# Performance work log

Hardware: AMD Instinct MI355X
Metric: run time of the kernel (lower is better)

The kernel has to match this reference:

```python
import jax, jax.numpy as jnp
import numpy as np

B, L, D, H = 8, 1024, 512, 8  # batch, seq, d_model, n_head (per-head dim == d_model)
EPS = 1e-6


def setup_inputs() -> dict:
    key = jax.random.key(0)
    ks = jax.random.split(key, 7)
    s = 1.0 / np.sqrt(D)
    return {
        "q": jax.random.normal(ks[0], (B, L, D), jnp.float32),
        "k": jax.random.normal(ks[1], (B, L, D), jnp.float32),
        "v": jax.random.normal(ks[2], (B, L, D), jnp.float32),
        "w_q": jax.random.normal(ks[3], (D, H * D), jnp.float32) * s,
        "w_k": jax.random.normal(ks[4], (D, H * D), jnp.float32) * s,
        "w_v": jax.random.normal(ks[5], (D, H * D), jnp.float32) * s,
        "w_fc": jax.random.normal(ks[6], (H * D, D), jnp.float32) * (1.0 / np.sqrt(H * D)),
        "ln_gamma": jnp.ones((D,), jnp.float32),
        "ln_beta": jnp.zeros((D,), jnp.float32),
    }


def reference(q, k, v, w_q, w_k, w_v, w_fc, ln_gamma, ln_beta):
    residual = q
    # projections -> (B, H, L, D); dropout is identity in eval mode
    qh = (q @ w_q).reshape(B, L, H, D).transpose(0, 2, 1, 3)
    kh = (k @ w_k).reshape(B, L, H, D).transpose(0, 2, 1, 3)
    vh = (v @ w_v).reshape(B, L, H, D).transpose(0, 2, 1, 3)
    temp = jnp.asarray(D, qh.dtype) ** 0.5
    scores = jnp.einsum("bhqd,bhkd->bhqk", qh / temp, kh)
    attn = jax.nn.softmax(scores, axis=-1)
    ctx = jnp.einsum("bhqk,bhkd->bhqd", attn, vh)
    ctx = ctx.transpose(0, 2, 1, 3).reshape(B, L, H * D)
    out = ctx @ w_fc + residual
    mu = jnp.mean(out, axis=-1, keepdims=True)
    var = jnp.var(out, axis=-1, keepdims=True)
    out = (out - mu) * jax.lax.rsqrt(var + EPS) * ln_gamma + ln_beta
    return out, attn
```

## Files before the change

### kernel.cpp

```cpp
#include <hip/hip_runtime.h>
#include <hip/hip_bf16.h>
#include <math.h>

typedef __bf16 bf16_t;
typedef __bf16 bf16x8 __attribute__((ext_vector_type(8)));
typedef __bf16 bf16x4 __attribute__((ext_vector_type(4)));
typedef float  f32x4  __attribute__((ext_vector_type(4)));

#define B_   8
#define L_   1024
#define D_   512
#define H_   8
#define HD_  4096
#define BL_  8192

__device__ __forceinline__ void gload_lds16(const bf16_t* g, bf16_t* l) {
  __builtin_amdgcn_global_load_lds(
      (const __attribute__((address_space(1))) unsigned int*)g,
      (__attribute__((address_space(3))) unsigned int*)l,
      16, 0, 0);
}

__global__ void f2b3(const float4* __restrict__ q, const float4* __restrict__ k,
                     const float4* __restrict__ v, bf16x4* __restrict__ qo,
                     bf16x4* __restrict__ ko, bf16x4* __restrict__ vo, int n4) {
  int i = blockIdx.x * blockDim.x + threadIdx.x;
  if (i >= n4) return;
  const float4* s = (blockIdx.y == 0) ? q : (blockIdx.y == 1) ? k : v;
  bf16x4* d = (blockIdx.y == 0) ? qo : (blockIdx.y == 1) ? ko : vo;
  float4 x = s[i];
  bf16x4 o;
  o[0] = (bf16_t)x.x; o[1] = (bf16_t)x.y; o[2] = (bf16_t)x.z; o[3] = (bf16_t)x.w;
  d[i] = o;
}

__global__ void tconv4(const float* __restrict__ wq, const float* __restrict__ wk,
                       const float* __restrict__ wv, const float* __restrict__ wfc,
                       bf16_t* __restrict__ wqT, bf16_t* __restrict__ wkT,
                       bf16_t* __restrict__ wvT, bf16_t* __restrict__ wfT) {
  __shared__ float t[32][33];
  const int z = blockIdx.z;
  const float* s; bf16_t* d; int R, C, c0, r0;
  if (z < 3) {
    s = (z == 0) ? wq : (z == 1) ? wk : wv;
    d = (z == 0) ? wqT : (z == 1) ? wkT : wvT;
    R = D_; C = HD_; c0 = blockIdx.x * 32; r0 = blockIdx.y * 32;
  } else {
    s = wfc; d = wfT;
    R = HD_; C = D_; c0 = blockIdx.y * 32; r0 = blockIdx.x * 32;
  }
  int tx = threadIdx.x, ty = threadIdx.y;
  #pragma unroll
  for (int i = 0; i < 32; i += 8)
    t[ty + i][tx] = s[(long)(r0 + ty + i) * C + c0 + tx];
  __syncthreads();
  #pragma unroll
  for (int i = 0; i < 32; i += 8)
    d[(long)(c0 + ty + i) * R + r0 + tx] = (bf16_t)t[tx][ty + i];
}

#define VM4 asm volatile("s_waitcnt vmcnt(4)" ::: "memory")
#define VM0 asm volatile("s_waitcnt vmcnt(0)" ::: "memory")

#define STG(OP, BUF, KK, TILE) do { \
  const bf16_t* gsrc_ = (OP) ? Bg : Ag; \
  const long gld_ = (OP) ? ldb : lda; \
  bf16_t* lb_ = lds + (BUF)*32768 + (OP)*16384 + (KK)*8192 + wid*512; \
  gload_lds16(gsrc_ + (long)(TILE)*64 + (KK)*32, lb_); \
  gload_lds16(gsrc_ + (long)128*gld_ + (long)(TILE)*64 + (KK)*32, lb_ + 4096); \
} while (0)

#define LDA(I, BUF, KK) (*(const bf16x8*)(lds + (BUF)*32768 + (KK)*8192 + offA[I]))
#define LDB(J, BUF, KK) (*(const bf16x8*)(lds + (BUF)*32768 + 16384 + (KK)*8192 + offB[J]))

#define MM(q, ii, jj) acc[(q)*4+(ii)][(jj)] = \
  __builtin_amdgcn_mfma_f32_16x16x32_bf16(a##ii, b##jj, acc[(q)*4+(ii)][(jj)], 0, 0, 0)

#define PHASE(Q, KK, BUF, STAGE, VM) do { \
  bf16x8 a0, a1, a2, a3; \
  if ((Q) == 0) { b0 = LDB(0,BUF,KK); b1 = LDB(1,BUF,KK); b2 = LDB(2,BUF,KK); b3 = LDB(3,BUF,KK); } \
  a0 = LDA((Q)*4+0,BUF,KK); a1 = LDA((Q)*4+1,BUF,KK); \
  a2 = LDA((Q)*4+2,BUF,KK); a3 = LDA((Q)*4+3,BUF,KK); \
  STAGE; \
  __builtin_amdgcn_s_barrier(); \
  asm volatile("s_waitcnt lgkmcnt(0)" ::: "memory"); \
  __builtin_amdgcn_sched_barrier(0); \
  __builtin_amdgcn_s_setprio(1); \
  MM(Q,0,0); MM(Q,1,0); MM(Q,2,0); MM(Q,3,0); \
  MM(Q,0,1); MM(Q,1,1); MM(Q,2,1); MM(Q,3,1); \
  MM(Q,0,2); MM(Q,1,2); MM(Q,2,2); MM(Q,3,2); \
  MM(Q,0,3); MM(Q,1,3); MM(Q,2,3); MM(Q,3,3); \
  __builtin_amdgcn_s_setprio(0); \
  VM; \
  __builtin_amdgcn_s_barrier(); \
} while (0)

template<int EPI>
__launch_bounds__(512, 2)
__global__ void gemm256(const bf16_t* __restrict__ A, long sAb, long sAh, int lda,
                        const bf16_t* __restrict__ Bt, long sBb, long sBh, int ldb,
                        void* __restrict__ Cv, long sCb, long sCh, int ldc,
                        int K, float scale)
{
  __shared__ __align__(16) bf16_t lds[65536];
  const int bz = blockIdx.z, b = bz >> 3, h = bz & 7;
  A  += (long)b * sAb + (long)h * sAh;
  Bt += (long)b * sBb + (long)h * sBh;
  const int m0 = blockIdx.y * 256, n0 = blockIdx.x * 256;
  const int tid = threadIdx.x, lane = tid & 63, wid = tid >> 6;
  const int wm = wid >> 2, wn = wid & 3;

  const int srow  = tid >> 2;
  const int sslot = (lane & 3) ^ ((tid >> 3) & 3);
  const bf16_t* Ag = A + (long)(m0 + srow) * lda + sslot * 8;
  const bf16_t* Bg = Bt + (long)(n0 + srow) * ldb + sslot * 8;

  int offA[8], offB[4];
  #pragma unroll
  for (int i = 0; i < 8; ++i) {
    const int r = wm * 128 + i * 16 + (lane & 15);
    offA[i] = r * 32 + (((lane >> 4) ^ ((r >> 1) & 3)) * 8);
  }
  #pragma unroll
  for (int j = 0; j < 4; ++j) {
    const int r = wn * 64 + j * 16 + (lane & 15);
    offB[j] = r * 32 + (((lane >> 4) ^ ((r >> 1) & 3)) * 8);
  }

  f32x4 acc[8][4] = {};
  const int ITER = K >> 7;

  STG(0,0,0,0); STG(0,0,1,0); STG(1,0,0,0); STG(1,0,1,0);
  STG(0,1,0,1); STG(1,1,0,1);
  VM4;
  __builtin_amdgcn_s_barrier();

  for (int i = 0; i < ITER; ++i) {
    const int t = 2 * i;
    const bool stg = (i + 1 < ITER);
    bf16x8 b0, b1, b2, b3;
    PHASE(0,0,0, STG(0,1,1,t+1);                , (void)0);
    PHASE(1,0,0, STG(1,1,1,t+1);                , (void)0);
    PHASE(0,1,0, { if (stg) STG(0,0,0,t+2); }   , (void)0);
    PHASE(1,1,0, { if (stg) STG(1,0,0,t+2); }   , { if (stg) { VM4; } else { VM0; } });
    PHASE(0,0,1, { if (stg) STG(0,0,1,t+2); }   , (void)0);
    PHASE(1,0,1, { if (stg) STG(1,0,1,t+2); }   , (void)0);
    PHASE(0,1,1, { if (stg) STG(0,1,0,t+3); }   , (void)0);
    PHASE(1,1,1, { if (stg) STG(1,1,0,t+3); }   , { if (stg) { VM4; } });
  }

  const long coff = (long)b * sCb + (long)h * sCh;
  #pragma unroll
  for (int i = 0; i < 8; ++i) {
    const int rbase = m0 + wm * 128 + i * 16 + ((lane >> 4) << 2);
    #pragma unroll
    for (int j = 0; j < 4; ++j) {
      const int c = n0 + wn * 64 + j * 16 + (lane & 15);
      if (EPI == 3) {
        const int b2 = rbase >> 10, l2 = rbase & 1023;
        const int h2 = c >> 9, d2 = c & 511;
        bf16x4 o4;
        #pragma unroll
        for (int r = 0; r < 4; ++r) o4[r] = (bf16_t)(acc[i][j][r] * scale);
        *(bf16x4*)((bf16_t*)Cv + (long)(b2 * 8 + h2) * D_ * L_ + (long)d2 * L_ + l2) = o4;
      } else {
        #pragma unroll
        for (int r = 0; r < 4; ++r) {
          float vv = acc[i][j][r] * scale;
          long idx = coff + (long)(rbase + r) * ldc + c;
          if (EPI == 0) ((bf16_t*)Cv)[idx] = (bf16_t)vv;
          else          ((float*)Cv)[idx] = vv;
        }
      }
    }
  }
}

template<int BM, int BN, int EPI>
__launch_bounds__(256, 2)
__global__ void gemm_bt(const bf16_t* __restrict__ A, long sAb, long sAh, int lda,
                        const bf16_t* __restrict__ Bt, long sBb, long sBh, int ldb,
                        void* __restrict__ Cv, long sCb, long sCh, int ldc,
                        int K, float scale, const float* __restrict__ res)
{
  constexpr int WN    = (BN == 128) ? 2 : 1;
  constexpr int SPANM = BM / (4 / WN);
  constexpr int MI    = SPANM / 16;
  constexpr int NJ    = 4;
  __shared__ bf16_t sA[BM * 64];
  __shared__ bf16_t sB[BN * 64];
  const int bz = blockIdx.z, b = bz >> 3, h = bz & 7;
  A  += (long)b * sAb + (long)h * sAh;
  Bt += (long)b * sBb + (long)h * sBh;
  const int m0 = blockIdx.y * BM, n0 = blockIdx.x * BN;
  const int tid = threadIdx.x, lane = tid & 63, wid = tid >> 6;
  const int waveM = (WN == 2) ? (wid >> 1) : wid;
  const int waveN = (WN == 2) ? (wid & 1) : 0;
  f32x4 acc[MI][NJ] = {};
  const int srow = wid * 8 + (lane >> 3);
  const int skin = (lane & 7) * 8;
  const bf16_t* Ag = A + (long)(m0 + srow) * lda + skin;
  const bf16_t* Bg = Bt + (long)(n0 + srow) * ldb + skin;
  for (int k0 = 0; k0 < K; k0 += 64) {
    #pragma unroll
    for (int j = 0; j < BM / 32; ++j)
      gload_lds16(Ag + (long)(j * 32) * lda + k0, sA + (j * 4 + wid) * 512);
    #pragma unroll
    for (int j = 0; j < BN / 32; ++j)
      gload_lds16(Bg + (long)(j * 32) * ldb + k0, sB + (j * 4 + wid) * 512);
    __syncthreads();
    #pragma unroll
    for (int kk = 0; kk < 2; ++kk) {
      bf16x8 af[MI], bfr[NJ];
      #pragma unroll
      for (int i = 0; i < MI; ++i)
        af[i]  = *(const bf16x8*)(sA + (waveM * SPANM + i * 16 + (lane & 15)) * 64 + kk * 32 + ((lane >> 4) * 8));
      #pragma unroll
      for (int j = 0; j < NJ; ++j)
        bfr[j] = *(const bf16x8*)(sB + (waveN * 64 + j * 16 + (lane & 15)) * 64 + kk * 32 + ((lane >> 4) * 8));
      #pragma unroll
      for (int i = 0; i < MI; ++i)
        #pragma unroll
        for (int j = 0; j < NJ; ++j)
          acc[i][j] = __builtin_amdgcn_mfma_f32_16x16x32_bf16(af[i], bfr[j], acc[i][j], 0, 0, 0);
    }
    __syncthreads();
  }
  const long coff = (long)b * sCb + (long)h * sCh;
  #pragma unroll
  for (int i = 0; i < MI; ++i) {
    const int rbase = m0 + waveM * SPANM + i * 16 + ((lane >> 4) << 2);
    #pragma unroll
    for (int j = 0; j < NJ; ++j) {
      const int c = n0 + waveN * 64 + j * 16 + (lane & 15);
      #pragma unroll
      for (int r = 0; r < 4; ++r) {
        float v = acc[i][j][r] * scale;
        long idx = coff + (long)(rbase + r) * ldc + c;
        if (EPI == 0)      ((bf16_t*)Cv)[idx] = (bf16_t)v;
        else if (EPI == 1) ((float*)Cv)[idx] = v;
        else               ((float*)Cv)[idx] = v + res[(long)(rbase + r) * ldc + c];
      }
    }
  }
}

__global__ void softmax_bf16(bf16_t* __restrict__ braw, float* __restrict__ attn) {
  const long row = (long)blockIdx.x * 4 + (threadIdx.x >> 6);
  const int lane = threadIdx.x & 63;
  bf16_t* p = braw + row * 1024;
  float* ao = attn + row * 1024;
  float v[16];
  float m = -1e30f;
  #pragma unroll
  for (int j = 0; j < 4; ++j) {
    bf16x4 x = *(const bf16x4*)(p + j * 256 + lane * 4);
    #pragma unroll
    for (int e = 0; e < 4; ++e) {
      v[j * 4 + e] = (float)x[e];
      m = fmaxf(m, v[j * 4 + e]);
    }
  }
  #pragma unroll
  for (int o = 32; o; o >>= 1) m = fmaxf(m, __shfl_xor(m, o));
  float s = 0.f;
  #pragma unroll
  for (int e = 0; e < 16; ++e) { v[e] = __expf(v[e] - m); s += v[e]; }
  #pragma unroll
  for (int o = 32; o; o >>= 1) s += __shfl_xor(s, o);
  const float inv = 1.f / s;
  #pragma unroll
  for (int j = 0; j < 4; ++j) {
    float4 f; bf16x4 o4;
    f.x = v[j*4+0] * inv; f.y = v[j*4+1] * inv;
    f.z = v[j*4+2] * inv; f.w = v[j*4+3] * inv;
    o4[0] = (bf16_t)f.x; o4[1] = (bf16_t)f.y; o4[2] = (bf16_t)f.z; o4[3] = (bf16_t)f.w;
    ((float4*)ao)[j * 64 + lane] = f;
    *(bf16x4*)(p + j * 256 + lane * 4) = o4;
  }
}

__global__ void softmax_rows(float* __restrict__ attn, bf16_t* __restrict__ abf) {
  const long row = (long)blockIdx.x * 4 + (threadIdx.x >> 6);
  const int lane = threadIdx.x & 63;
  float* p = attn + row * 1024;
  float4 v[4];
  float m = -1e30f;
  #pragma unroll
  for (int j = 0; j < 4; ++j) {
    v[j] = ((const float4*)p)[j * 64 + lane];
    m = fmaxf(m, fmaxf(fmaxf(v[j].x, v[j].y), fmaxf(v[j].z, v[j].w)));
  }
  #pragma unroll
  for (int o = 32; o; o >>= 1) m = fmaxf(m, __shfl_xor(m, o));
  float s = 0.f;
  #pragma unroll
  for (int j = 0; j < 4; ++j) {
    v[j].x = expf(v[j].x - m); v[j].y = expf(v[j].y - m);
    v[j].z = expf(v[j].z - m); v[j].w = expf(v[j].w - m);
    s += v[j].x + v[j].y + v[j].z + v[j].w;
  }
  #pragma unroll
  for (int o = 32; o; o >>= 1) s += __shfl_xor(s, o);
  const float inv = 1.f / s;
  bf16x4* ab = (bf16x4*)(abf + row * 1024);
  #pragma unroll
  for (int j = 0; j < 4; ++j) {
    v[j].x *= inv; v[j].y *= inv; v[j].z *= inv; v[j].w *= inv;
    ((float4*)p)[j * 64 + lane] = v[j];
    bf16x4 o4;
    o4[0] = (bf16_t)v[j].x; o4[1] = (bf16_t)v[j].y;
    o4[2] = (bf16_t)v[j].z; o4[3] = (bf16_t)v[j].w;
    ab[j * 64 + lane] = o4;
  }
}

__global__ void ln_rows(float* __restrict__ o, const float* __restrict__ g,
                        const float* __restrict__ be) {
  const long row = (long)blockIdx.x * 4 + (threadIdx.x >> 6);
  const int lane = threadIdx.x & 63;
  float* p = o + row * 512;
  float4 a = ((const float4*)p)[lane];
  float4 b = ((const float4*)p)[lane + 64];
  float s  = a.x + a.y + a.z + a.w + b.x + b.y + b.z + b.w;
  float s2 = a.x*a.x + a.y*a.y + a.z*a.z + a.w*a.w
           + b.x*b.x + b.y*b.y + b.z*b.z + b.w*b.w;
  #pragma unroll
  for (int t = 32; t; t >>= 1) { s += __shfl_xor(s, t); s2 += __shfl_xor(s2, t); }
  const float mu  = s * (1.f / 512.f);
  const float var = s2 * (1.f / 512.f) - mu * mu;
  const float inv = rsqrtf(var + 1e-6f);
  float4 g0 = ((const float4*)g)[lane],  g1 = ((const float4*)g)[lane + 64];
  float4 b0 = ((const float4*)be)[lane], b1 = ((const float4*)be)[lane + 64];
  a.x = (a.x - mu) * inv * g0.x + b0.x;  a.y = (a.y - mu) * inv * g0.y + b0.y;
  a.z = (a.z - mu) * inv * g0.z + b0.z;  a.w = (a.w - mu) * inv * g0.w + b0.w;
  b.x = (b.x - mu) * inv * g1.x + b1.x;  b.y = (b.y - mu) * inv * g1.y + b1.y;
  b.z = (b.z - mu) * inv * g1.z + b1.z;  b.w = (b.w - mu) * inv * g1.w + b1.w;
  ((float4*)p)[lane] = a;
  ((float4*)p)[lane + 64] = b;
}

extern "C" void kernel_launch(void* const* d_in, const int* in_sizes, int n_in,
                              void* d_out, int out_size, void* d_ws, size_t ws_size,
                              hipStream_t stream) {
  const float* q   = (const float*)d_in[0];
  const float* k   = (const float*)d_in[1];
  const float* v   = (const float*)d_in[2];
  const float* wq  = (const float*)d_in[3];
  const float* wk  = (const float*)d_in[4];
  const float* wv  = (const float*)d_in[5];
  const float* wfc = (const float*)d_in[6];
  const float* lng = (const float*)d_in[7];
  const float* lnb = (const float*)d_in[8];

  float* out   = (float*)d_out;
  float* attnf = out + (long)BL_ * D_;

  char* ws = (char*)d_ws;
  const long MB = 1024 * 1024;
  bf16_t* qbf = (bf16_t*)(ws +   0 * MB);
  bf16_t* kbf = (bf16_t*)(ws +   8 * MB);
  bf16_t* vbf = (bf16_t*)(ws +  16 * MB);
  bf16_t* wqT = (bf16_t*)(ws +  24 * MB);
  bf16_t* wkT = (bf16_t*)(ws +  28 * MB);
  bf16_t* wvT = (bf16_t*)(ws +  32 * MB);
  bf16_t* wfT = (bf16_t*)(ws +  36 * MB);
  bf16_t* qh  = (bf16_t*)(ws +  40 * MB);
  bf16_t* kh  = (bf16_t*)(ws + 104 * MB);
  bf16_t* vh  = (bf16_t*)(ws + 168 * MB);
  bf16_t* vhT = (bf16_t*)(ws + 232 * MB);
  bf16_t* ctx = vh;

  const bool fused = (ws_size >= (size_t)(424 * MB));
  bf16_t* braw = (bf16_t*)(ws + 296 * MB);
  bf16_t* abf  = fused ? braw : qh;

  const int n4 = BL_ * D_ / 4;
  f2b3<<<dim3(n4 / 256, 3), 256, 0, stream>>>((const float4*)q, (const float4*)k,
                                              (const float4*)v, (bf16x4*)qbf,
                                              (bf16x4*)kbf, (bf16x4*)vbf, n4);
  tconv4<<<dim3(128, 16, 4), dim3(32, 8), 0, stream>>>(wq, wk, wv, wfc,
                                                       wqT, wkT, wvT, wfT);

  const float qscale = 1.0f / sqrtf((float)D_);
  gemm256<0><<<dim3(16, 32, 1), 512, 0, stream>>>(qbf, 0, 0, D_, wqT, 0, 0, D_,
                                                  qh, 0, 0, HD_, D_, qscale);
  gemm256<0><<<dim3(16, 32, 1), 512, 0, stream>>>(kbf, 0, 0, D_, wkT, 0, 0, D_,
                                                  kh, 0, 0, HD_, D_, 1.0f);
  gemm256<3><<<dim3(16, 32, 1), 512, 0, stream>>>(vbf, 0, 0, D_, wvT, 0, 0, D_,
                                                  vhT, 0, 0, 0, D_, 1.0f);

  if (fused) {
    gemm256<0><<<dim3(4, 4, B_ * H_), 512, 0, stream>>>(
        qh, (long)L_ * HD_, D_, HD_,
        kh, (long)L_ * HD_, D_, HD_,
        braw, (long)H_ * L_ * L_, (long)L_ * L_, L_, D_, 1.0f);
    softmax_bf16<<<dim3(B_ * H_ * L_ / 4), 256, 0, stream>>>(braw, attnf);
  } else {
    gemm256<1><<<dim3(4, 4, B_ * H_), 512, 0, stream>>>(
        qh, (long)L_ * HD_, D_, HD_,
        kh, (long)L_ * HD_, D_, HD_,
        attnf, (long)H_ * L_ * L_, (long)L_ * L_, L_, D_, 1.0f);
    softmax_rows<<<dim3(B_ * H_ * L_ / 4), 256, 0, stream>>>(attnf, abf);
  }

  gemm256<0><<<dim3(2, 4, B_ * H_), 512, 0, stream>>>(
      abf, (long)H_ * L_ * L_, (long)L_ * L_, L_,
      vhT, (long)H_ * D_ * L_, (long)D_ * L_, L_,
      ctx, (long)L_ * HD_, D_, HD_, L_, 1.0f);

  gemm_bt<128,64,2><<<dim3(8, 64, 1), 256, 0, stream>>>(
      ctx, 0, 0, HD_, wfT, 0, 0, HD_,
      out, 0, 0, D_, HD_, 1.0f, q);

  ln_rows<<<dim3(BL_ / 4), 256, 0, stream>>>(out, lng, lnb);
}
```

Baseline: 565.4 us.

## Fuse Q/K/V projection GEMMs into one launch and remap blocks across XCDs

Replaces the three separate Q, K and V projection GEMM launches with a single 48x32 grid. The column tile index selects the input, the weight slice and the output layout, and the V part keeps its transposed epilogue. This relies on the input and output buffers being laid out contiguously. It also adds an XCD-aware block-index remap to both GEMM kernels, so neighbouring tiles land on the same chiplet and share L2, and removes the now-unused EPI 3 path. The aim is to cut launch overhead and tail waste, at the cost of branchier epilogue code and hard-coded buffer offsets.

New measurement: 558.3 us, median of 2. No clear change (-1.2%).

```diff
diff --git a/kernel.cpp b/kernel.cpp
--- a/kernel.cpp
+++ b/kernel.cpp
@@ -13,12 +13,23 @@
 #define H_   8
 #define HD_  4096
 #define BL_  8192
+#define KOFF 33554432L
 
 __device__ __forceinline__ void gload_lds16(const bf16_t* g, bf16_t* l) {
   __builtin_amdgcn_global_load_lds(
       (const __attribute__((address_space(1))) unsigned int*)g,
       (__attribute__((address_space(3))) unsigned int*)l,
       16, 0, 0);
+}
+
+__device__ __forceinline__ void xcd_remap(int& tx, int& ty, int& tz) {
+  const int nwg = gridDim.x * gridDim.y * gridDim.z;
+  const int lin = blockIdx.x + gridDim.x * (blockIdx.y + gridDim.y * blockIdx.z);
+  const int virt = (lin & 7) * (nwg >> 3) + (lin >> 3);
+  tx = virt % gridDim.x;
+  const int rem = virt / gridDim.x;
+  ty = rem % gridDim.y;
+  tz = rem / gridDim.y;
 }
 
 __global__ void f2b3(const float4* __restrict__ q, const float4* __restrict__ k,
@@ -100,13 +111,19 @@
 __global__ void gemm256(const bf16_t* __restrict__ A, long sAb, long sAh, int lda,
                         const bf16_t* __restrict__ Bt, long sBb, long sBh, int ldb,
                         void* __restrict__ Cv, long sCb, long sCh, int ldc,
-                        int K, float scale)
+                        int K, float scale, void* __restrict__ Cv2)
 {
   __shared__ __align__(16) bf16_t lds[65536];
-  const int bz = blockIdx.z, b = bz >> 3, h = bz & 7;
-  A  += (long)b * sAb + (long)h * sAh;
+  int tx, ty, tz;
+  xcd_remap(tx, ty, tz);
+  const int bz = tz, b = bz >> 3, h = bz & 7;
+  if (EPI == 4) {
+    A += (long)((tx >= 32) ? 2 : (tx >= 16) ? 1 : 0) * sAb;
+  } else {
+    A += (long)b * sAb + (long)h * sAh;
+  }
   Bt += (long)b * sBb + (long)h * sBh;
-  const int m0 = blockIdx.y * 256, n0 = blockIdx.x * 256;
+  const int m0 = ty * 256, n0 = tx * 256;
   const int tid = threadIdx.x, lane = tid & 63, wid = tid >> 6;
   const int wm = wid >> 2, wn = wid & 3;
 
@@ -149,6 +166,7 @@
     PHASE(1,1,1, { if (stg) STG(1,1,0,t+3); }   , { if (stg) { VM4; } });
   }
 
+  const float sc = (EPI == 4 && tx >= 16) ? 1.0f : scale;
   const long coff = (long)b * sCb + (long)h * sCh;
   #pragma unroll
   for (int i = 0; i < 8; ++i) {
@@ -156,17 +174,26 @@
     #pragma unroll
     for (int j = 0; j < 4; ++j) {
       const int c = n0 + wn * 64 + j * 16 + (lane & 15);
-      if (EPI == 3) {
-        const int b2 = rbase >> 10, l2 = rbase & 1023;
-        const int h2 = c >> 9, d2 = c & 511;
-        bf16x4 o4;
-        #pragma unroll
-        for (int r = 0; r < 4; ++r) o4[r] = (bf16_t)(acc[i][j][r] * scale);
-        *(bf16x4*)((bf16_t*)Cv + (long)(b2 * 8 + h2) * D_ * L_ + (long)d2 * L_ + l2) = o4;
+      if (EPI == 4) {
+        if (tx < 32) {
+          bf16_t* dst = (bf16_t*)Cv + (tx >= 16 ? KOFF : 0);
+          const int cc = c - (tx >= 16 ? 4096 : 0);
+          #pragma unroll
+          for (int r = 0; r < 4; ++r)
+            dst[(long)(rbase + r) * HD_ + cc] = (bf16_t)(acc[i][j][r] * sc);
+        } else {
+          const int cc = c - 8192;
+          const int b2 = rbase >> 10, l2 = rbase & 1023;
+          const int h2 = cc >> 9, d2 = cc & 511;
+          bf16x4 o4;
+          #pragma unroll
+          for (int r = 0; r < 4; ++r) o4[r] = (bf16_t)acc[i][j][r];
+          *(bf16x4*)((bf16_t*)Cv2 + (long)(b2 * 8 + h2) * D_ * L_ + (long)d2 * L_ + l2) = o4;
+        }
       } else {
         #pragma unroll
         for (int r = 0; r < 4; ++r) {
-          float vv = acc[i][j][r] * scale;
+          float vv = acc[i][j][r] * sc;
           long idx = coff + (long)(rbase + r) * ldc + c;
           if (EPI == 0) ((bf16_t*)Cv)[idx] = (bf16_t)vv;
           else          ((float*)Cv)[idx] = vv;
@@ -189,10 +216,12 @@
   constexpr int NJ    = 4;
   __shared__ bf16_t sA[BM * 64];
   __shared__ bf16_t sB[BN * 64];
-  const int bz = blockIdx.z, b = bz >> 3, h = bz & 7;
+  int tx, ty, tz;
+  xcd_remap(tx, ty, tz);
+  const int bz = tz, b = bz >> 3, h = bz & 7;
   A  += (long)b * sAb + (long)h * sAh;
   Bt += (long)b * sBb + (long)h * sBh;
-  const int m0 = blockIdx.y * BM, n0 = blockIdx.x * BN;
+  const int m0 = ty * BM, n0 = tx * BN;
   const int tid = threadIdx.x, lane = tid & 63, wid = tid >> 6;
   const int waveM = (WN == 2) ? (wid >> 1) : wid;
   const int waveN = (WN == 2) ? (wid & 1) : 0;
@@ -383,31 +412,28 @@
                                                        wqT, wkT, wvT, wfT);
 
   const float qscale = 1.0f / sqrtf((float)D_);
-  gemm256<0><<<dim3(16, 32, 1), 512, 0, stream>>>(qbf, 0, 0, D_, wqT, 0, 0, D_,
-                                                  qh, 0, 0, HD_, D_, qscale);
-  gemm256<0><<<dim3(16, 32, 1), 512, 0, stream>>>(kbf, 0, 0, D_, wkT, 0, 0, D_,
-                                                  kh, 0, 0, HD_, D_, 1.0f);
-  gemm256<3><<<dim3(16, 32, 1), 512, 0, stream>>>(vbf, 0, 0, D_, wvT, 0, 0, D_,
-                                                  vhT, 0, 0, 0, D_, 1.0f);
+  gemm256<4><<<dim3(48, 32, 1), 512, 0, stream>>>(qbf, 4194304L, 0, D_,
+                                                  wqT, 0, 0, D_,
+                                                  qh, 0, 0, HD_, D_, qscale, vhT);
 
   if (fused) {
     gemm256<0><<<dim3(4, 4, B_ * H_), 512, 0, stream>>>(
         qh, (long)L_ * HD_, D_, HD_,
         kh, (long)L_ * HD_, D_, HD_,
-        braw, (long)H_ * L_ * L_, (long)L_ * L_, L_, D_, 1.0f);
+        braw, (long)H_ * L_ * L_, (long)L_ * L_, L_, D_, 1.0f, nullptr);
     softmax_bf16<<<dim3(B_ * H_ * L_ / 4), 256, 0, stream>>>(braw, attnf);
   } else {
     gemm256<1><<<dim3(4, 4, B_ * H_), 512, 0, stream>>>(
         qh, (long)L_ * HD_, D_, HD_,
         kh, (long)L_ * HD_, D_, HD_,
-        attnf, (long)H_ * L_ * L_, (long)L_ * L_, L_, D_, 1.0f);
+        attnf, (long)H_ * L_ * L_, (long)L_ * L_, L_, D_, 1.0f, nullptr);
     softmax_rows<<<dim3(B_ * H_ * L_ / 4), 256, 0, stream>>>(attnf, abf);
   }
 
   gemm256<0><<<dim3(2, 4, B_ * H_), 512, 0, stream>>>(
       abf, (long)H_ * L_ * L_, (long)L_ * L_, L_,
       vhT, (long)H_ * D_ * L_, (long)D_ * L_, L_,
-      ctx, (long)L_ * HD_, D_, HD_, L_, 1.0f);
+      ctx, (long)L_ * HD_, D_, HD_, L_, 1.0f, nullptr);
 
   gemm_bt<128,64,2><<<dim3(8, 64, 1), 256, 0, stream>>>(
       ctx, 0, 0, HD_, wfT, 0, 0, HD_,
```
